# Performance work log

Hardware: AMD Instinct MI355X
Metric: run time of the kernel (lower is better)

## Reference

```python
import jax, jax.numpy as jnp
import numpy as np
from functools import partial

# Gate order along axis 0 of Wi/bi/Wh/bh: 0=r (input gate), 1=f (forget), 2=g (cell), 3=o (output)

def setup_inputs() -> dict:
    key = jax.random.key(0)
    ks = jax.random.split(key, 6)
    B, T, V, E, H, O = 64, 512, 32000, 256, 512, 1
    s_e, s_h = 1.0 / np.sqrt(E), 1.0 / np.sqrt(H)
    return {
        "input_words": jax.random.randint(ks[0], (B, T), 0, V, dtype=jnp.int64),
        "emb": jax.random.normal(ks[1], (V, E), dtype=jnp.float32) * 0.02,
        "Wi": jax.random.normal(ks[2], (4, H, E), dtype=jnp.float32) * s_e,
        "bi": jnp.zeros((4, H), dtype=jnp.float32),
        "Wh": jax.random.normal(ks[3], (4, H, H), dtype=jnp.float32) * s_h,
        "bh": jnp.zeros((4, H), dtype=jnp.float32),
        "Wfc": jax.random.normal(ks[4], (O, H), dtype=jnp.float32) * s_h,
        "bfc": jnp.zeros((O,), dtype=jnp.float32),
    }


def reference(input_words, emb, Wi, bi, Wh, bh, Wfc, bfc):
    B, T = input_words.shape
    H = Wh.shape[-1]
    x = emb[input_words]                     # [B, T, E]
    # Precompute input projections for all 4 gates, all timesteps: one big GEMM.
    xg = jnp.einsum('bte,ghe->tbgh', x, Wi) + bi  # [T, B, 4, H]

    def step(carry, xg_t):
        h, c = carry
        gates = xg_t + jnp.einsum('bk,ghk->bgh', h, Wh) + bh  # [B, 4, H]
        r = jax.nn.sigmoid(gates[:, 0])
        f = jax.nn.sigmoid(gates[:, 1])
        g = jnp.tanh(gates[:, 2])
        o = jax.nn.sigmoid(gates[:, 3])
        c = f * c + r * g
        h = o * jnp.tanh(c)
        return (h, c), None

    h0 = jnp.zeros((B, H), dtype=x.dtype)
    c0 = jnp.zeros((B, H), dtype=x.dtype)
    (h, c), _ = jax.lax.scan(step, (h0, c0), xg)
    out = jax.nn.sigmoid(h @ Wfc.T + bfc)    # [B, n_output]
    return (out, h)
```

## Files before the change

kernel.cpp:

```cpp
#include <hip/hip_runtime.h>
#include <hip/hip_bf16.h>

#define TB 512
#define NB 64
#define EE 256
#define HH 512
#define ND 8
#define DB 8
#define NBLK 8
#define NT 256
#define NCOLP 260
#define NPAIR 256
#define GCOLS 2048
#define SLOWOFF ((size_t)0x40000)
#define XGOFF   ((size_t)1 << 20)

typedef __bf16 bf16_t;
typedef bf16_t bf16x8 __attribute__((ext_vector_type(8)));
typedef float  f32x4  __attribute__((ext_vector_type(4)));
typedef unsigned u32;
typedef unsigned long long u64;
typedef u32 u32x4 __attribute__((ext_vector_type(4)));

__device__ __forceinline__ float sigf(float x) { return 1.0f / (1.0f + __expf(-x)); }
__device__ __forceinline__ float tanhfast(float x) {
    float xc = fminf(fmaxf(x, -15.0f), 15.0f);
    float e  = __expf(2.0f * xc);
    return (e - 1.0f) / (e + 1.0f);
}
__device__ __forceinline__ u32 bfbits(float f) {
    bf16_t h = (bf16_t)f;
    return (u32)__builtin_bit_cast(unsigned short, h);
}
__device__ __forceinline__ bf16x8 cvt8(float4 a, float4 b) {
    bf16x8 v;
    v[0]=(bf16_t)a.x; v[1]=(bf16_t)a.y; v[2]=(bf16_t)a.z; v[3]=(bf16_t)a.w;
    v[4]=(bf16_t)b.x; v[5]=(bf16_t)b.y; v[6]=(bf16_t)b.z; v[7]=(bf16_t)b.w;
    return v;
}
__device__ __forceinline__ f32x4 cvtxg(u64 v) {
    f32x4 r;
    r[0] = __uint_as_float((u32)( v        & 0xFFFFu) << 16);
    r[1] = __uint_as_float((u32)((v >> 16) & 0xFFFFu) << 16);
    r[2] = __uint_as_float((u32)((v >> 32) & 0xFFFFu) << 16);
    r[3] = __uint_as_float((u32)((v >> 48) & 0xFFFFu) << 16);
    return r;
}

__device__ __forceinline__ void poll8_dual(const u64* fsrc, const u64* ssrc,
                                           u32 tag, u64 (&pk)[4]) {
    u64 fa = (u64)fsrc;
    int it = 0;
    for (;;) {
        u32x4 q0, q1, q2, q3;
        asm volatile(
            "global_load_dwordx4 %0, %4, off sc0\n\t"
            "global_load_dwordx4 %1, %4, off offset:16 sc0\n\t"
            "global_load_dwordx4 %2, %4, off offset:32 sc0\n\t"
            "global_load_dwordx4 %3, %4, off offset:48 sc0\n\t"
            "s_waitcnt vmcnt(0)"
            : "=&v"(q0), "=&v"(q1), "=&v"(q2), "=&v"(q3)
            : "v"(fa)
            : "memory");
        if (q0[1]==tag && q0[3]==tag && q1[1]==tag && q1[3]==tag &&
            q2[1]==tag && q2[3]==tag && q3[1]==tag && q3[3]==tag) {
            pk[0] = (u64)q0[0] | ((u64)q0[2] << 32);
            pk[1] = (u64)q1[0] | ((u64)q1[2] << 32);
            pk[2] = (u64)q2[0] | ((u64)q2[2] << 32);
            pk[3] = (u64)q3[0] | ((u64)q3[2] << 32);
            return;
        }
        if (((++it) & 1) == 0) {
            u64 hv[8];
            #pragma unroll
            for (int j = 0; j < 8; ++j)
                hv[j] = __hip_atomic_load(ssrc + j, __ATOMIC_RELAXED, __HIP_MEMORY_SCOPE_AGENT);
            bool ok = true;
            #pragma unroll
            for (int j = 0; j < 8; ++j) ok &= ((u32)(hv[j] >> 32) == tag);
            if (ok) {
                #pragma unroll
                for (int k = 0; k < 4; ++k)
                    pk[k] = (u64)(u32)hv[2*k] | ((u64)(u32)hv[2*k + 1] << 32);
                return;
            }
        }
    }
}

__global__ __launch_bounds__(256, 1)
void xg_prepass(const int* __restrict__ words, const float* __restrict__ emb,
                const float* __restrict__ Wi, const float* __restrict__ bi,
                const float* __restrict__ bh, bf16_t* __restrict__ xgT)
{
    const int tid = threadIdx.x, lane = tid & 63, wv = tid >> 6;
    const int kgrp = lane >> 4, cl = lane & 15;
    const int cc = blockIdx.x & 7, tc = blockIdx.x >> 3;

    __shared__ __align__(16) bf16_t x_s[64][EE];

    bf16x8 wf[8][4];
    float  bv[4];
    #pragma unroll
    for (int nt = 0; nt < 4; ++nt) {
        int col = cc*256 + wv*64 + nt*16 + cl;
        int wrow = (col & 3)*HH + (col >> 2);
        const float* wr = Wi + (size_t)wrow*EE;
        #pragma unroll
        for (int kt = 0; kt < 8; ++kt) {
            const float4* p = (const float4*)(wr + kt*32 + kgrp*8);
            wf[kt][nt] = cvt8(p[0], p[1]);
        }
        bv[nt] = bi[wrow] + bh[wrow];
    }

    const int r0 = tid >> 2, q = tid & 3;
    const int swz = (r0 & 7) << 3;
    u64* dst = (u64*)xgT;

    for (int it = 0; it < 16; ++it) {
        int t = tc*16 + it;
        {
            int wd = words[r0*TB + t];
            const float4* p = (const float4*)(emb + (size_t)wd*EE + q*64);
            #pragma unroll
            for (int o = 0; o < 8; ++o) {
                float4 a = p[2*o], b2 = p[2*o + 1];
                *(bf16x8*)&x_s[r0][(q*64 + o*8) ^ swz] = cvt8(a, b2);
            }
        }
        __syncthreads();

        f32x4 acc[4][4];
        #pragma unroll
        for (int rt = 0; rt < 4; ++rt)
            #pragma unroll
            for (int nt = 0; nt < 4; ++nt)
                acc[rt][nt] = (f32x4){ bv[nt], bv[nt], bv[nt], bv[nt] };
        #pragma unroll
        for (int kt = 0; kt < 8; ++kt) {
            #pragma unroll
            for (int rt = 0; rt < 4; ++rt) {
                bf16x8 a = *(const bf16x8*)&x_s[rt*16 + cl][(kt*32 + kgrp*8) ^ ((cl & 7) << 3)];
                #pragma unroll
                for (int nt = 0; nt < 4; ++nt)
                    acc[rt][nt] = __builtin_amdgcn_mfma_f32_16x16x32_bf16(a, wf[kt][nt], acc[rt][nt], 0, 0, 0);
            }
        }
        #pragma unroll
        for (int nt = 0; nt < 4; ++nt) {
            int col = cc*256 + wv*64 + nt*16 + cl;
            #pragma unroll
            for (int rt = 0; rt < 4; ++rt) {
                f32x4 v = acc[rt][nt];
                u64 pkk =  (u64)(bfbits(v[0]))
                        | ((u64)(bfbits(v[1])) << 16)
                        | ((u64)(bfbits(v[2])) << 32)
                        | ((u64)(bfbits(v[3])) << 48);
                dst[(size_t)(t*GCOLS + col)*16 + rt*4 + kgrp] = pkk;
            }
        }
        __syncthreads();
    }
}

__global__ __launch_bounds__(NT, 1)
void lstm_main(const float* __restrict__ Wh,
               const float* __restrict__ Wfc,
               const float* __restrict__ bfc,
               float* __restrict__ out,
               u64* __restrict__ fastH,
               u64* __restrict__ slowH,
               const u64* __restrict__ xg64)
{
    const int tid  = threadIdx.x;
    const int lane = tid & 63;
    const int wv   = tid >> 6;
    const int g    = blockIdx.x >> 3;
    const int ug   = blockIdx.x & 7;
    const int kgrp = lane >> 4;
    const int cl   = lane & 15;

    __shared__ __align__(16) bf16_t h_lds[16][HH];
    __shared__ __align__(16) float  P_lds[16][NCOLP];

    for (int i = tid; i < 16*HH/2; i += NT) ((u32*)h_lds)[i] = 0u;

    bf16x8 whf[16][4];
    #pragma unroll
    for (int nt = 0; nt < 4; ++nt) {
        int gc = ug*256 + wv*64 + nt*16 + cl;
        int wrow = (gc & 3)*HH + (gc >> 2);
        const float* wr = Wh + (size_t)wrow*HH;
        #pragma unroll
        for (int kt = 0; kt < 16; ++kt) {
            const float4* p = (const float4*)(wr + kt*32 + kgrp*8);
            whf[kt][nt] = cvt8(p[0], p[1]);
        }
    }

    const int sb = tid >> 5, sc = tid & 31;
    const int swz = sb << 3;

    const int m = 2*g + (kgrp & 1);
    int gc[4];
    #pragma unroll
    for (int nt = 0; nt < 4; ++nt) gc[nt] = ug*256 + wv*64 + nt*16 + cl;

    u64 xgc[4], xgn[4];
    #pragma unroll
    for (int nt = 0; nt < 4; ++nt) xgc[nt] = xg64[(size_t)gc[nt]*16 + m];

    float c0 = 0.f, c1 = 0.f;
    __syncthreads();

    for (int t = 0; t < TB; ++t) {
        if (t > 0) {
            size_t off = ((size_t)((t & 1) ^ 1))*NB*NPAIR
                       + (size_t)(g*DB + sb)*NPAIR + sc*8;
            u64 pk[4];
            poll8_dual(fastH + off, slowH + off, (u32)t, pk);
            #pragma unroll
            for (int k = 0; k < 4; ++k) {
                int e = sc*16 + 4*k;
                int phys = ((e & ~7) ^ swz) | (e & 7);
                *(u64*)&h_lds[sb][phys] = pk[k];
            }
        }

        if (t + 1 < TB) {
            #pragma unroll
            for (int nt = 0; nt < 4; ++nt)
                xgn[nt] = xg64[(size_t)((t + 1)*GCOLS + gc[nt])*16 + m];
        }
        __syncthreads();

        f32x4 acc[4];
        #pragma unroll
        for (int nt = 0; nt < 4; ++nt) acc[nt] = cvtxg(xgc[nt]);
        if (t > 0) {
            #pragma unroll
            for (int kt = 0; kt < 16; ++kt) {
                bf16x8 a = *(const bf16x8*)&h_lds[cl][(kt*32 + kgrp*8) ^ ((cl & 7) << 3)];
                #pragma unroll
                for (int nt = 0; nt < 4; ++nt)
                    acc[nt] = __builtin_amdgcn_mfma_f32_16x16x32_bf16(a, whf[kt][nt], acc[nt], 0, 0, 0);
            }
        }

        #pragma unroll
        for (int nt = 0; nt < 4; ++nt)
            #pragma unroll
            for (int r = 0; r < 4; ++r)
                P_lds[kgrp*4 + r][wv*64 + nt*16 + cl] = acc[nt][r];
        __syncthreads();

        {
            float4 g0 = *(const float4*)&P_lds[sb][sc*8];
            float4 g1 = *(const float4*)&P_lds[sb][sc*8 + 4];
            float r0 = sigf(g0.x), f0 = sigf(g0.y), z0 = tanhfast(g0.z), o0 = sigf(g0.w);
            float r1 = sigf(g1.x), f1 = sigf(g1.y), z1 = tanhfast(g1.z), o1 = sigf(g1.w);
            c0 = f0*c0 + r0*z0;
            c1 = f1*c1 + r1*z1;
            float h0 = o0*tanhfast(c0);
            float h1 = o1*tanhfast(c1);
            if (t == TB - 1) {
                float2 hw = { h0, h1 };
                *(float2*)&out[64 + (size_t)(g*DB + sb)*HH + ug*64 + 2*sc] = hw;
            }
            u64 v = (((u64)(u32)(t + 1)) << 32)
                  | (u64)(bfbits(h0) | (bfbits(h1) << 16));
            size_t di = ((size_t)(t & 1))*NB*NPAIR
                      + (size_t)(g*DB + sb)*NPAIR + ug*32 + sc;
            asm volatile("global_store_dwordx2 %0, %1, off sc0"
                         :: "v"((u64)(fastH + di)), "v"(v) : "memory");
            __hip_atomic_store(slowH + di, v, __ATOMIC_RELAXED, __HIP_MEMORY_SCOPE_AGENT);
        }
        #pragma unroll
        for (int nt = 0; nt < 4; ++nt) xgc[nt] = xgn[nt];
    }

    if (ug == 0) {
        size_t off = ((size_t)((TB - 1) & 1))*NB*NPAIR
                   + (size_t)(g*DB + sb)*NPAIR + sc*8;
        u64 pk[4];
        poll8_dual(fastH + off, slowH + off, (u32)TB, pk);
        float s = 0.f;
        const float4* wp = (const float4*)(Wfc + sc*16);
        #pragma unroll
        for (int k = 0; k < 4; ++k) {
            float4 w = wp[k];
            u64 p = pk[k];
            s += __uint_as_float((u32)( p        & 0xFFFFu) << 16) * w.x;
            s += __uint_as_float((u32)((p >> 16) & 0xFFFFu) << 16) * w.y;
            s += __uint_as_float((u32)((p >> 32) & 0xFFFFu) << 16) * w.z;
            s += __uint_as_float((u32)((p >> 48) & 0xFFFFu) << 16) * w.w;
        }
        __syncthreads();
        P_lds[sb][sc] = s;
        __syncthreads();
        if (tid < 8) {
            float acc = 0.f;
            #pragma unroll
            for (int q = 0; q < 32; ++q) acc += P_lds[tid][q];
            out[g*DB + tid] = sigf(acc + bfc[0]);
        }
    }
}

extern "C" void kernel_launch(void* const* d_in, const int* in_sizes, int n_in,
                              void* d_out, int out_size, void* d_ws, size_t ws_size,
                              hipStream_t stream) {
    (void)in_sizes; (void)n_in; (void)out_size; (void)ws_size;
    const int*   words = (const int*)d_in[0];
    const float* emb   = (const float*)d_in[1];
    const float* Wi    = (const float*)d_in[2];
    const float* bi    = (const float*)d_in[3];
    const float* Wh    = (const float*)d_in[4];
    const float* bh    = (const float*)d_in[5];
    const float* Wfc   = (const float*)d_in[6];
    const float* bfc   = (const float*)d_in[7];
    float* out = (float*)d_out;

    u64* fastH  = (u64*)d_ws;
    u64* slowH  = (u64*)((char*)d_ws + SLOWOFF);
    bf16_t* xgT = (bf16_t*)((char*)d_ws + XGOFF);

    hipMemsetAsync(d_ws, 0, 2*SLOWOFF, stream);

    xg_prepass<<<dim3(256), dim3(256), 0, stream>>>(words, emb, Wi, bi, bh, xgT);
    lstm_main<<<dim3(ND*NBLK), dim3(NT), 0, stream>>>(Wh, Wfc, bfc, out,
                                                      fastH, slowH, (const u64*)xgT);
}
```

Before: 2.144 ms.

## Replace per-thread tagged polling with per-block sentinel flags polled by one wave

```diff
diff --git a/kernel.cpp b/kernel.cpp
--- a/kernel.cpp
+++ b/kernel.cpp
@@ -13,6 +13,7 @@
 #define NPAIR 256
 #define GCOLS 2048
 #define SLOWOFF ((size_t)0x40000)
+#define SENTOFF ((size_t)0x80000)
 #define XGOFF   ((size_t)1 << 20)
 
 typedef __bf16 bf16_t;
@@ -47,10 +48,9 @@
     return r;
 }
 
-__device__ __forceinline__ void poll8_dual(const u64* fsrc, const u64* ssrc,
-                                           u32 tag, u64 (&pk)[4]) {
+__device__ __forceinline__ void read8_tagged(const u64* fsrc, const u64* ssrc,
+                                             u32 tag, u64 (&pk)[4]) {
     u64 fa = (u64)fsrc;
-    int it = 0;
     for (;;) {
         u32x4 q0, q1, q2, q3;
         asm volatile(
@@ -70,20 +70,18 @@
             pk[3] = (u64)q3[0] | ((u64)q3[2] << 32);
             return;
         }
-        if (((++it) & 1) == 0) {
-            u64 hv[8];
-            #pragma unroll
-            for (int j = 0; j < 8; ++j)
-                hv[j] = __hip_atomic_load(ssrc + j, __ATOMIC_RELAXED, __HIP_MEMORY_SCOPE_AGENT);
-            bool ok = true;
-            #pragma unroll
-            for (int j = 0; j < 8; ++j) ok &= ((u32)(hv[j] >> 32) == tag);
-            if (ok) {
-                #pragma unroll
-                for (int k = 0; k < 4; ++k)
-                    pk[k] = (u64)(u32)hv[2*k] | ((u64)(u32)hv[2*k + 1] << 32);
-                return;
-            }
+        u64 hv[8];
+        #pragma unroll
+        for (int j = 0; j < 8; ++j)
+            hv[j] = __hip_atomic_load(ssrc + j, __ATOMIC_RELAXED, __HIP_MEMORY_SCOPE_AGENT);
+        bool ok = true;
+        #pragma unroll
+        for (int j = 0; j < 8; ++j) ok &= ((u32)(hv[j] >> 32) == tag);
+        if (ok) {
+            #pragma unroll
+            for (int k = 0; k < 4; ++k)
+                pk[k] = (u64)(u32)hv[2*k] | ((u64)(u32)hv[2*k + 1] << 32);
+            return;
         }
     }
 }
@@ -171,6 +169,7 @@
                float* __restrict__ out,
                u64* __restrict__ fastH,
                u64* __restrict__ slowH,
+               u64* __restrict__ sent,
                const u64* __restrict__ xg64)
 {
     const int tid  = threadIdx.x;
@@ -181,6 +180,9 @@
     const int kgrp = lane >> 4;
     const int cl   = lane & 15;
 
+    u64* sentF = sent;
+    u64* sentS = sent + 64*8;
+
     __shared__ __align__(16) bf16_t h_lds[16][HH];
     __shared__ __align__(16) float  P_lds[16][NCOLP];
 
@@ -216,10 +218,32 @@
 
     for (int t = 0; t < TB; ++t) {
         if (t > 0) {
+            if (wv == 0) {
+                const bool ml = (lane < 8);
+                const u64 sfa = (u64)(sentF + (size_t)(g*8 + (lane & 7))*8);
+                const u64* ssp = sentS + (size_t)(g*8 + (lane & 7))*8;
+                int it = 0;
+                for (;;) {
+                    u64 v = 0;
+                    if (ml) {
+                        if (it & 1) {
+                            asm volatile("global_load_dwordx2 %0, %1, off sc0\n\t"
+                                         "s_waitcnt vmcnt(0)"
+                                         : "=v"(v) : "v"(sfa) : "memory");
+                        } else {
+                            v = __hip_atomic_load(ssp, __ATOMIC_RELAXED, __HIP_MEMORY_SCOPE_AGENT);
+                        }
+                    }
+                    if (__all(ml ? (int)(v >= (u64)t) : 1)) break;
+                    ++it;
+                }
+            }
+            __syncthreads();
+
             size_t off = ((size_t)((t & 1) ^ 1))*NB*NPAIR
                        + (size_t)(g*DB + sb)*NPAIR + sc*8;
             u64 pk[4];
-            poll8_dual(fastH + off, slowH + off, (u32)t, pk);
+            read8_tagged(fastH + off, slowH + off, (u32)t, pk);
             #pragma unroll
             for (int k = 0; k < 4; ++k) {
                 int e = sc*16 + 4*k;
@@ -276,15 +300,48 @@
                          :: "v"((u64)(fastH + di)), "v"(v) : "memory");
             __hip_atomic_store(slowH + di, v, __ATOMIC_RELAXED, __HIP_MEMORY_SCOPE_AGENT);
         }
+
+        __builtin_amdgcn_sched_barrier(0);
+        asm volatile("s_waitcnt vmcnt(0)" ::: "memory");
+        __builtin_amdgcn_sched_barrier(0);
+        __syncthreads();
+        if (tid == NT - 1) {
+            u64 sv = (u64)(t + 1);
+            asm volatile("global_store_dwordx2 %0, %1, off sc0"
+                         :: "v"((u64)(sentF + (size_t)blockIdx.x*8)), "v"(sv) : "memory");
+            __hip_atomic_store(sentS + (size_t)blockIdx.x*8, sv,
+                               __ATOMIC_RELAXED, __HIP_MEMORY_SCOPE_AGENT);
+        }
         #pragma unroll
         for (int nt = 0; nt < 4; ++nt) xgc[nt] = xgn[nt];
     }
 
     if (ug == 0) {
+        if (wv == 0) {
+            const bool ml = (lane < 8);
+            const u64 sfa = (u64)(sentF + (size_t)(g*8 + (lane & 7))*8);
+            const u64* ssp = sentS + (size_t)(g*8 + (lane & 7))*8;
+            int it = 0;
+            for (;;) {
+                u64 v = 0;
+                if (ml) {
+                    if (it & 1) {
+                        asm volatile("global_load_dwordx2 %0, %1, off sc0\n\t"
+                                     "s_waitcnt vmcnt(0)"
+                                     : "=v"(v) : "v"(sfa) : "memory");
+                    } else {
+                        v = __hip_atomic_load(ssp, __ATOMIC_RELAXED, __HIP_MEMORY_SCOPE_AGENT);
+                    }
+                }
+                if (__all(ml ? (int)(v >= (u64)TB) : 1)) break;
+                ++it;
+            }
+        }
+        __syncthreads();
         size_t off = ((size_t)((TB - 1) & 1))*NB*NPAIR
                    + (size_t)(g*DB + sb)*NPAIR + sc*8;
         u64 pk[4];
-        poll8_dual(fastH + off, slowH + off, (u32)TB, pk);
+        read8_tagged(fastH + off, slowH + off, (u32)TB, pk);
         float s = 0.f;
         const float4* wp = (const float4*)(Wfc + sc*16);
         #pragma unroll
@@ -324,11 +381,12 @@
 
     u64* fastH  = (u64*)d_ws;
     u64* slowH  = (u64*)((char*)d_ws + SLOWOFF);
+    u64* sent   = (u64*)((char*)d_ws + SENTOFF);
     bf16_t* xgT = (bf16_t*)((char*)d_ws + XGOFF);
 
-    hipMemsetAsync(d_ws, 0, 2*SLOWOFF, stream);
+    hipMemsetAsync(d_ws, 0, SENTOFF + 2*64*8*sizeof(u64), stream);
 
     xg_prepass<<<dim3(256), dim3(256), 0, stream>>>(words, emb, Wi, bi, bh, xgT);
     lstm_main<<<dim3(ND*NBLK), dim3(NT), 0, stream>>>(Wh, Wfc, bfc, out,
-                                                      fastH, slowH, (const u64*)xgT);
-}
+                                                      fastH, slowH, sent, (const u64*)xgT);
+}
```

Result: slower. 2.521 ms (+17.6%).

## Load h fragments directly from global into MFMA operands, 16 batches per block

Applied to the files above, without the earlier changes.

```diff
diff --git a/kernel.cpp b/kernel.cpp
--- a/kernel.cpp
+++ b/kernel.cpp
@@ -5,8 +5,8 @@
 #define NB 64
 #define EE 256
 #define HH 512
-#define ND 8
-#define DB 8
+#define ND 4
+#define DB 16
 #define NBLK 8
 #define NT 256
 #define NCOLP 260
@@ -47,43 +47,56 @@
     return r;
 }
 
-__device__ __forceinline__ void poll8_dual(const u64* fsrc, const u64* ssrc,
-                                           u32 tag, u64 (&pk)[4]) {
-    u64 fa = (u64)fsrc;
-    int it = 0;
-    for (;;) {
-        u32x4 q0, q1, q2, q3;
-        asm volatile(
-            "global_load_dwordx4 %0, %4, off sc0\n\t"
-            "global_load_dwordx4 %1, %4, off offset:16 sc0\n\t"
-            "global_load_dwordx4 %2, %4, off offset:32 sc0\n\t"
-            "global_load_dwordx4 %3, %4, off offset:48 sc0\n\t"
-            "s_waitcnt vmcnt(0)"
-            : "=&v"(q0), "=&v"(q1), "=&v"(q2), "=&v"(q3)
-            : "v"(fa)
-            : "memory");
-        if (q0[1]==tag && q0[3]==tag && q1[1]==tag && q1[3]==tag &&
-            q2[1]==tag && q2[3]==tag && q3[1]==tag && q3[3]==tag) {
-            pk[0] = (u64)q0[0] | ((u64)q0[2] << 32);
-            pk[1] = (u64)q1[0] | ((u64)q1[2] << 32);
-            pk[2] = (u64)q2[0] | ((u64)q2[2] << 32);
-            pk[3] = (u64)q3[0] | ((u64)q3[2] << 32);
-            return;
-        }
-        if (((++it) & 1) == 0) {
-            u64 hv[8];
-            #pragma unroll
-            for (int j = 0; j < 8; ++j)
-                hv[j] = __hip_atomic_load(ssrc + j, __ATOMIC_RELAXED, __HIP_MEMORY_SCOPE_AGENT);
-            bool ok = true;
-            #pragma unroll
-            for (int j = 0; j < 8; ++j) ok &= ((u32)(hv[j] >> 32) == tag);
-            if (ok) {
-                #pragma unroll
-                for (int k = 0; k < 4; ++k)
-                    pk[k] = (u64)(u32)hv[2*k] | ((u64)(u32)hv[2*k + 1] << 32);
-                return;
-            }
+__device__ __forceinline__ void bar_lds() {
+    __builtin_amdgcn_sched_barrier(0);
+    asm volatile("s_waitcnt lgkmcnt(0)" ::: "memory");
+    __builtin_amdgcn_s_barrier();
+    __builtin_amdgcn_sched_barrier(0);
+}
+
+__device__ __forceinline__ void frag_issue(u64 fa, u32x4 (&q)[8]) {
+    asm volatile(
+        "global_load_dwordx4 %0, %8, off sc0\n\t"
+        "global_load_dwordx4 %1, %8, off offset:16 sc0\n\t"
+        "global_load_dwordx4 %2, %8, off offset:128 sc0\n\t"
+        "global_load_dwordx4 %3, %8, off offset:144 sc0\n\t"
+        "global_load_dwordx4 %4, %8, off offset:256 sc0\n\t"
+        "global_load_dwordx4 %5, %8, off offset:272 sc0\n\t"
+        "global_load_dwordx4 %6, %8, off offset:384 sc0\n\t"
+        "global_load_dwordx4 %7, %8, off offset:400 sc0"
+        : "=&v"(q[0]), "=&v"(q[1]), "=&v"(q[2]), "=&v"(q[3]),
+          "=&v"(q[4]), "=&v"(q[5]), "=&v"(q[6]), "=&v"(q[7])
+        : "v"(fa)
+        : "memory");
+}
+
+__device__ __forceinline__ bool frag_wait_ok(u32x4 (&q)[8], u32 tag) {
+    asm volatile("s_waitcnt vmcnt(0)"
+        : "+v"(q[0]), "+v"(q[1]), "+v"(q[2]), "+v"(q[3]),
+          "+v"(q[4]), "+v"(q[5]), "+v"(q[6]), "+v"(q[7])
+        :: "memory");
+    __builtin_amdgcn_sched_barrier(0);
+    bool ok = true;
+    #pragma unroll
+    for (int i = 0; i < 8; ++i) ok &= (q[i][1] == tag) & (q[i][3] == tag);
+    return ok;
+}
+
+__device__ __forceinline__ void frag_get(u64 fa, const u64* sb, u32 tag, u32x4 (&q)[8]) {
+    int round = 0;
+    while (!frag_wait_ok(q, tag)) {
+        if ((round++ & 1) == 0) {
+            #pragma unroll
+            for (int j = 0; j < 4; ++j) {
+                u64 h0 = __hip_atomic_load(sb + j*16 + 0, __ATOMIC_RELAXED, __HIP_MEMORY_SCOPE_AGENT);
+                u64 h1 = __hip_atomic_load(sb + j*16 + 1, __ATOMIC_RELAXED, __HIP_MEMORY_SCOPE_AGENT);
+                u64 h2 = __hip_atomic_load(sb + j*16 + 2, __ATOMIC_RELAXED, __HIP_MEMORY_SCOPE_AGENT);
+                u64 h3 = __hip_atomic_load(sb + j*16 + 3, __ATOMIC_RELAXED, __HIP_MEMORY_SCOPE_AGENT);
+                q[2*j]   = (u32x4){(u32)h0, (u32)(h0 >> 32), (u32)h1, (u32)(h1 >> 32)};
+                q[2*j+1] = (u32x4){(u32)h2, (u32)(h2 >> 32), (u32)h3, (u32)(h3 >> 32)};
+            }
+        } else {
+            frag_issue(fa, q);
         }
     }
 }
@@ -181,10 +194,7 @@
     const int kgrp = lane >> 4;
     const int cl   = lane & 15;
 
-    __shared__ __align__(16) bf16_t h_lds[16][HH];
-    __shared__ __align__(16) float  P_lds[16][NCOLP];
-
-    for (int i = tid; i < 16*HH/2; i += NT) ((u32*)h_lds)[i] = 0u;
+    __shared__ __align__(16) float P_lds[16][NCOLP];
 
     bf16x8 whf[16][4];
     #pragma unroll
@@ -199,52 +209,58 @@
         }
     }
 
-    const int sb = tid >> 5, sc = tid & 31;
-    const int swz = sb << 3;
-
-    const int m = 2*g + (kgrp & 1);
-    int gc[4];
-    #pragma unroll
-    for (int nt = 0; nt < 4; ++nt) gc[nt] = ug*256 + wv*64 + nt*16 + cl;
+    const int m = g*4 + kgrp;
+    int gcv[4];
+    #pragma unroll
+    for (int nt = 0; nt < 4; ++nt) gcv[nt] = ug*256 + wv*64 + nt*16 + cl;
 
     u64 xgc[4], xgn[4];
     #pragma unroll
-    for (int nt = 0; nt < 4; ++nt) xgc[nt] = xg64[(size_t)gc[nt]*16 + m];
-
-    float c0 = 0.f, c1 = 0.f;
+    for (int nt = 0; nt < 4; ++nt) xgc[nt] = xg64[(size_t)gcv[nt]*16 + m];
+
+    const int ab = tid >> 4, us = tid & 15;
+    float cs0 = 0.f, cs1 = 0.f, cs2 = 0.f, cs3 = 0.f;
+
     __syncthreads();
 
     for (int t = 0; t < TB; ++t) {
+        if (t + 1 < TB) {
+            #pragma unroll
+            for (int nt = 0; nt < 4; ++nt)
+                xgn[nt] = xg64[(size_t)((t + 1)*GCOLS + gcv[nt])*16 + m];
+        }
+
+        f32x4 acc[4];
+        #pragma unroll
+        for (int nt = 0; nt < 4; ++nt) acc[nt] = cvtxg(xgc[nt]);
+
         if (t > 0) {
-            size_t off = ((size_t)((t & 1) ^ 1))*NB*NPAIR
-                       + (size_t)(g*DB + sb)*NPAIR + sc*8;
-            u64 pk[4];
-            poll8_dual(fastH + off, slowH + off, (u32)t, pk);
-            #pragma unroll
-            for (int k = 0; k < 4; ++k) {
-                int e = sc*16 + 4*k;
-                int phys = ((e & ~7) ^ swz) | (e & 7);
-                *(u64*)&h_lds[sb][phys] = pk[k];
-            }
-        }
-
-        if (t + 1 < TB) {
-            #pragma unroll
-            for (int nt = 0; nt < 4; ++nt)
-                xgn[nt] = xg64[(size_t)((t + 1)*GCOLS + gc[nt])*16 + m];
-        }
-        __syncthreads();
-
-        f32x4 acc[4];
-        #pragma unroll
-        for (int nt = 0; nt < 4; ++nt) acc[nt] = cvtxg(xgc[nt]);
-        if (t > 0) {
-            #pragma unroll
-            for (int kt = 0; kt < 16; ++kt) {
-                bf16x8 a = *(const bf16x8*)&h_lds[cl][(kt*32 + kgrp*8) ^ ((cl & 7) << 3)];
+            size_t poff = ((size_t)((t & 1) ^ 1))*NB*NPAIR + (size_t)(g*DB + cl)*NPAIR;
+            const u64* fb  = fastH + poff;
+            const u64* sb2 = slowH + poff;
+            u32x4 q[8];
+            frag_issue((u64)fb*1 + (size_t)kgrp*32 + 0, q);
+            #pragma unroll
+            for (int grp = 0; grp < 4; ++grp) {
+                u64 fa = (u64)fb + (size_t)grp*512 + (size_t)kgrp*32;
+                frag_get(fa, sb2 + grp*64 + kgrp*4, (u32)t, q);
+                bf16x8 af[4];
+                union U { u32 w[4]; bf16x8 v; };
+                {
+                    U u0; u0.w[0]=q[0][0]; u0.w[1]=q[0][2]; u0.w[2]=q[1][0]; u0.w[3]=q[1][2]; af[0]=u0.v;
+                    U u1; u1.w[0]=q[2][0]; u1.w[1]=q[2][2]; u1.w[2]=q[3][0]; u1.w[3]=q[3][2]; af[1]=u1.v;
+                    U u2; u2.w[0]=q[4][0]; u2.w[1]=q[4][2]; u2.w[2]=q[5][0]; u2.w[3]=q[5][2]; af[2]=u2.v;
+                    U u3; u3.w[0]=q[6][0]; u3.w[1]=q[6][2]; u3.w[2]=q[7][0]; u3.w[3]=q[7][2]; af[3]=u3.v;
+                }
+                if (grp < 3)
+                    frag_issue((u64)fb + (size_t)(grp + 1)*512 + (size_t)kgrp*32, q);
                 #pragma unroll
-                for (int nt = 0; nt < 4; ++nt)
-                    acc[nt] = __builtin_amdgcn_mfma_f32_16x16x32_bf16(a, whf[kt][nt], acc[nt], 0, 0, 0);
+                for (int j = 0; j < 4; ++j) {
+                    int kt = grp*4 + j;
+                    #pragma unroll
+                    for (int nt = 0; nt < 4; ++nt)
+                        acc[nt] = __builtin_amdgcn_mfma_f32_16x16x32_bf16(af[j], whf[kt][nt], acc[nt], 0, 0, 0);
+                }
             }
         }
 
@@ -253,56 +269,72 @@
             #pragma unroll
             for (int r = 0; r < 4; ++r)
                 P_lds[kgrp*4 + r][wv*64 + nt*16 + cl] = acc[nt][r];
+        bar_lds();
+
+        {
+            float4 p0 = *(const float4*)&P_lds[ab][us*16 + 0];
+            float4 p1 = *(const float4*)&P_lds[ab][us*16 + 4];
+            float4 p2 = *(const float4*)&P_lds[ab][us*16 + 8];
+            float4 p3 = *(const float4*)&P_lds[ab][us*16 + 12];
+            float h0, h1, h2, h3;
+            { float r=sigf(p0.x), f=sigf(p0.y), z=tanhfast(p0.z), o=sigf(p0.w);
+              cs0 = f*cs0 + r*z; h0 = o*tanhfast(cs0); }
+            { float r=sigf(p1.x), f=sigf(p1.y), z=tanhfast(p1.z), o=sigf(p1.w);
+              cs1 = f*cs1 + r*z; h1 = o*tanhfast(cs1); }
+            { float r=sigf(p2.x), f=sigf(p2.y), z=tanhfast(p2.z), o=sigf(p2.w);
+              cs2 = f*cs2 + r*z; h2 = o*tanhfast(cs2); }
+            { float r=sigf(p3.x), f=sigf(p3.y), z=tanhfast(p3.z), o=sigf(p3.w);
+              cs3 = f*cs3 + r*z; h3 = o*tanhfast(cs3); }
+            if (t == TB - 1) {
+                float4 hw = { h0, h1, h2, h3 };
+                *(float4*)&out[64 + (size_t)(g*DB + ab)*HH + ug*64 + us*4] = hw;
+            }
+            u64 tg = ((u64)(u32)(t + 1)) << 32;
+            u64 v0 = tg | (u64)(bfbits(h0) | (bfbits(h1) << 16));
+            u64 v1 = tg | (u64)(bfbits(h2) | (bfbits(h3) << 16));
+            size_t di = ((size_t)(t & 1))*NB*NPAIR
+                      + (size_t)(g*DB + ab)*NPAIR + ug*32 + us*2;
+            asm volatile(
+                "global_store_dwordx2 %0, %1, off sc0\n\t"
+                "global_store_dwordx2 %0, %2, off offset:8 sc0"
+                :: "v"((u64)(fastH + di)), "v"(v0), "v"(v1) : "memory");
+            __hip_atomic_store(slowH + di,     v0, __ATOMIC_RELAXED, __HIP_MEMORY_SCOPE_AGENT);
+            __hip_atomic_store(slowH + di + 1, v1, __ATOMIC_RELAXED, __HIP_MEMORY_SCOPE_AGENT);
+        }
+        bar_lds();
+        #pragma unroll
+        for (int nt = 0; nt < 4; ++nt) xgc[nt] = xgn[nt];
+    }
+
+    if (ug == 0) {
         __syncthreads();
-
-        {
-            float4 g0 = *(const float4*)&P_lds[sb][sc*8];
-            float4 g1 = *(const float4*)&P_lds[sb][sc*8 + 4];
-            float r0 = sigf(g0.x), f0 = sigf(g0.y), z0 = tanhfast(g0.z), o0 = sigf(g0.w);
-            float r1 = sigf(g1.x), f1 = sigf(g1.y), z1 = tanhfast(g1.z), o1 = sigf(g1.w);
-            c0 = f0*c0 + r0*z0;
-            c1 = f1*c1 + r1*z1;
-            float h0 = o0*tanhfast(c0);
-            float h1 = o1*tanhfast(c1);
-            if (t == TB - 1) {
-                float2 hw = { h0, h1 };
-                *(float2*)&out[64 + (size_t)(g*DB + sb)*HH + ug*64 + 2*sc] = hw;
-            }
-            u64 v = (((u64)(u32)(t + 1)) << 32)
-                  | (u64)(bfbits(h0) | (bfbits(h1) << 16));
-            size_t di = ((size_t)(t & 1))*NB*NPAIR
-                      + (size_t)(g*DB + sb)*NPAIR + ug*32 + sc;
-            asm volatile("global_store_dwordx2 %0, %1, off sc0"
-                         :: "v"((u64)(fastH + di)), "v"(v) : "memory");
-            __hip_atomic_store(slowH + di, v, __ATOMIC_RELAXED, __HIP_MEMORY_SCOPE_AGENT);
-        }
-        #pragma unroll
-        for (int nt = 0; nt < 4; ++nt) xgc[nt] = xgn[nt];
-    }
-
-    if (ug == 0) {
-        size_t off = ((size_t)((TB - 1) & 1))*NB*NPAIR
-                   + (size_t)(g*DB + sb)*NPAIR + sc*8;
-        u64 pk[4];
-        poll8_dual(fastH + off, slowH + off, (u32)TB, pk);
+        int b = tid >> 4, seg = tid & 15;
+        const u64* sp = slowH + (size_t)1*NB*NPAIR + (size_t)(g*DB + b)*NPAIR + seg*16;
+        u64 hv[16];
+        for (;;) {
+            bool ok = true;
+            #pragma unroll
+            for (int j = 0; j < 16; ++j) {
+                hv[j] = __hip_atomic_load(sp + j, __ATOMIC_RELAXED, __HIP_MEMORY_SCOPE_AGENT);
+                ok &= ((u32)(hv[j] >> 32) == (u32)TB);
+            }
+            if (ok) break;
+            __builtin_amdgcn_s_sleep(1);
+        }
         float s = 0.f;
-        const float4* wp = (const float4*)(Wfc + sc*16);
-        #pragma unroll
-        for (int k = 0; k < 4; ++k) {
-            float4 w = wp[k];
-            u64 p = pk[k];
-            s += __uint_as_float((u32)( p        & 0xFFFFu) << 16) * w.x;
-            s += __uint_as_float((u32)((p >> 16) & 0xFFFFu) << 16) * w.y;
-            s += __uint_as_float((u32)((p >> 32) & 0xFFFFu) << 16) * w.z;
-            s += __uint_as_float((u32)((p >> 48) & 0xFFFFu) << 16) * w.w;
-        }
+        #pragma unroll
+        for (int j = 0; j < 16; ++j) {
+            u32 pl = (u32)hv[j];
+            int u = seg*32 + 2*j;
+            s += __uint_as_float((pl & 0xFFFFu) << 16) * Wfc[u];
+            s += __uint_as_float(pl & 0xFFFF0000u)     * Wfc[u + 1];
+        }
+        P_lds[b][seg] = s;
         __syncthreads();
-        P_lds[sb][sc] = s;
-        __syncthreads();
-        if (tid < 8) {
+        if (tid < 16) {
             float acc = 0.f;
             #pragma unroll
-            for (int q = 0; q < 32; ++q) acc += P_lds[tid][q];
+            for (int q2 = 0; q2 < 16; ++q2) acc += P_lds[tid][q2];
             out[g*DB + tid] = sigf(acc + bfc[0]);
         }
     }
```

Measured after the change: 6.497 ms. +203.0%, slower.

## Split LSTM block into compute and polling waves with double-buffered h

Applied to the files above, without the earlier changes.

```diff
diff --git a/kernel.cpp b/kernel.cpp
--- a/kernel.cpp
+++ b/kernel.cpp
@@ -8,7 +8,7 @@
 #define ND 8
 #define DB 8
 #define NBLK 8
-#define NT 256
+#define NT 512
 #define NCOLP 260
 #define NPAIR 256
 #define GCOLS 2048
@@ -45,6 +45,13 @@
     r[2] = __uint_as_float((u32)((v >> 32) & 0xFFFFu) << 16);
     r[3] = __uint_as_float((u32)((v >> 48) & 0xFFFFu) << 16);
     return r;
+}
+
+__device__ __forceinline__ void bar_lds() {
+    __builtin_amdgcn_sched_barrier(0);
+    asm volatile("s_waitcnt lgkmcnt(0)" ::: "memory");
+    __builtin_amdgcn_s_barrier();
+    __builtin_amdgcn_sched_barrier(0);
 }
 
 __device__ __forceinline__ void poll8_dual(const u64* fsrc, const u64* ssrc,
@@ -70,7 +77,7 @@
             pk[3] = (u64)q3[0] | ((u64)q3[2] << 32);
             return;
         }
-        if (((++it) & 1) == 0) {
+        if (((++it) & 3) == 0) {
             u64 hv[8];
             #pragma unroll
             for (int j = 0; j < 8; ++j)
@@ -176,20 +183,22 @@
     const int tid  = threadIdx.x;
     const int lane = tid & 63;
     const int wv   = tid >> 6;
+    const int wvm  = wv & 3;
     const int g    = blockIdx.x >> 3;
     const int ug   = blockIdx.x & 7;
     const int kgrp = lane >> 4;
     const int cl   = lane & 15;
-
-    __shared__ __align__(16) bf16_t h_lds[16][HH];
+    const bool cw  = (wv < 4);
+
+    __shared__ __align__(16) bf16_t h_lds[2][16][HH];
     __shared__ __align__(16) float  P_lds[16][NCOLP];
 
-    for (int i = tid; i < 16*HH/2; i += NT) ((u32*)h_lds)[i] = 0u;
+    for (int i = tid; i < 2*16*HH/2; i += NT) ((u32*)h_lds)[i] = 0u;
 
     bf16x8 whf[16][4];
     #pragma unroll
     for (int nt = 0; nt < 4; ++nt) {
-        int gc = ug*256 + wv*64 + nt*16 + cl;
+        int gc = ug*256 + wvm*64 + nt*16 + cl;
         int wrow = (gc & 3)*HH + (gc >> 2);
         const float* wr = Wh + (size_t)wrow*HH;
         #pragma unroll
@@ -199,63 +208,49 @@
         }
     }
 
-    const int sb = tid >> 5, sc = tid & 31;
-    const int swz = sb << 3;
+    const int sb = (tid >> 5) & 7, sc = tid & 31;
+    const int io  = tid - 256;
+    const int iob = (io >> 5) & 7, ioc = io & 31;
+    const int ioswz = (iob & 7) << 3;
 
     const int m = 2*g + (kgrp & 1);
-    int gc[4];
+    int gcv[4];
     #pragma unroll
-    for (int nt = 0; nt < 4; ++nt) gc[nt] = ug*256 + wv*64 + nt*16 + cl;
-
-    u64 xgc[4], xgn[4];
-    #pragma unroll
-    for (int nt = 0; nt < 4; ++nt) xgc[nt] = xg64[(size_t)gc[nt]*16 + m];
+    for (int nt = 0; nt < 4; ++nt) gcv[nt] = ug*256 + wvm*64 + nt*16 + cl;
+
+    u64 xgc[4] = {0,0,0,0}, xgn[4] = {0,0,0,0};
+    if (cw) {
+        #pragma unroll
+        for (int nt = 0; nt < 4; ++nt) xgc[nt] = xg64[(size_t)gcv[nt]*16 + m];
+    }
 
     float c0 = 0.f, c1 = 0.f;
     __syncthreads();
 
     for (int t = 0; t < TB; ++t) {
-        if (t > 0) {
-            size_t off = ((size_t)((t & 1) ^ 1))*NB*NPAIR
-                       + (size_t)(g*DB + sb)*NPAIR + sc*8;
-            u64 pk[4];
-            poll8_dual(fastH + off, slowH + off, (u32)t, pk);
-            #pragma unroll
-            for (int k = 0; k < 4; ++k) {
-                int e = sc*16 + 4*k;
-                int phys = ((e & ~7) ^ swz) | (e & 7);
-                *(u64*)&h_lds[sb][phys] = pk[k];
-            }
-        }
-
-        if (t + 1 < TB) {
+        if (cw) {
+            f32x4 acc[4];
+            #pragma unroll
+            for (int nt = 0; nt < 4; ++nt) acc[nt] = cvtxg(xgc[nt]);
+            if (t > 0) {
+                const bf16_t (*hb)[HH] = h_lds[(t & 1) ^ 1];
+                #pragma unroll
+                for (int kt = 0; kt < 16; ++kt) {
+                    bf16x8 a = *(const bf16x8*)&hb[cl][(kt*32 + kgrp*8) ^ ((cl & 7) << 3)];
+                    #pragma unroll
+                    for (int nt = 0; nt < 4; ++nt)
+                        acc[nt] = __builtin_amdgcn_mfma_f32_16x16x32_bf16(a, whf[kt][nt], acc[nt], 0, 0, 0);
+                }
+            }
             #pragma unroll
             for (int nt = 0; nt < 4; ++nt)
-                xgn[nt] = xg64[(size_t)((t + 1)*GCOLS + gc[nt])*16 + m];
-        }
-        __syncthreads();
-
-        f32x4 acc[4];
-        #pragma unroll
-        for (int nt = 0; nt < 4; ++nt) acc[nt] = cvtxg(xgc[nt]);
-        if (t > 0) {
-            #pragma unroll
-            for (int kt = 0; kt < 16; ++kt) {
-                bf16x8 a = *(const bf16x8*)&h_lds[cl][(kt*32 + kgrp*8) ^ ((cl & 7) << 3)];
-                #pragma unroll
-                for (int nt = 0; nt < 4; ++nt)
-                    acc[nt] = __builtin_amdgcn_mfma_f32_16x16x32_bf16(a, whf[kt][nt], acc[nt], 0, 0, 0);
-            }
-        }
-
-        #pragma unroll
-        for (int nt = 0; nt < 4; ++nt)
-            #pragma unroll
-            for (int r = 0; r < 4; ++r)
-                P_lds[kgrp*4 + r][wv*64 + nt*16 + cl] = acc[nt][r];
-        __syncthreads();
-
-        {
+                #pragma unroll
+                for (int r = 0; r < 4; ++r)
+                    P_lds[kgrp*4 + r][wvm*64 + nt*16 + cl] = acc[nt][r];
+        }
+        bar_lds();
+
+        if (cw) {
             float4 g0 = *(const float4*)&P_lds[sb][sc*8];
             float4 g1 = *(const float4*)&P_lds[sb][sc*8 + 4];
             float r0 = sigf(g0.x), f0 = sigf(g0.y), z0 = tanhfast(g0.z), o0 = sigf(g0.w);
@@ -275,34 +270,63 @@
             asm volatile("global_store_dwordx2 %0, %1, off sc0"
                          :: "v"((u64)(fastH + di)), "v"(v) : "memory");
             __hip_atomic_store(slowH + di, v, __ATOMIC_RELAXED, __HIP_MEMORY_SCOPE_AGENT);
-        }
-        #pragma unroll
-        for (int nt = 0; nt < 4; ++nt) xgc[nt] = xgn[nt];
+            if (t + 1 < TB) {
+                #pragma unroll
+                for (int nt = 0; nt < 4; ++nt)
+                    xgn[nt] = xg64[(size_t)((t + 1)*GCOLS + gcv[nt])*16 + m];
+            }
+            #pragma unroll
+            for (int nt = 0; nt < 4; ++nt) xgc[nt] = xgn[nt];
+        } else if (t + 1 < TB) {
+            size_t off = ((size_t)(t & 1))*NB*NPAIR
+                       + (size_t)(g*DB + iob)*NPAIR + ioc*8;
+            u64 pk[4];
+            poll8_dual(fastH + off, slowH + off, (u32)(t + 1), pk);
+            #pragma unroll
+            for (int k = 0; k < 4; ++k) {
+                int e = ioc*16 + 4*k;
+                int phys = ((e & ~7) ^ ioswz) | (e & 7);
+                *(u64*)&h_lds[t & 1][iob][phys] = pk[k];
+            }
+        }
+        bar_lds();
     }
 
     if (ug == 0) {
-        size_t off = ((size_t)((TB - 1) & 1))*NB*NPAIR
-                   + (size_t)(g*DB + sb)*NPAIR + sc*8;
-        u64 pk[4];
-        poll8_dual(fastH + off, slowH + off, (u32)TB, pk);
         float s = 0.f;
-        const float4* wp = (const float4*)(Wfc + sc*16);
-        #pragma unroll
-        for (int k = 0; k < 4; ++k) {
-            float4 w = wp[k];
-            u64 p = pk[k];
-            s += __uint_as_float((u32)( p        & 0xFFFFu) << 16) * w.x;
-            s += __uint_as_float((u32)((p >> 16) & 0xFFFFu) << 16) * w.y;
-            s += __uint_as_float((u32)((p >> 32) & 0xFFFFu) << 16) * w.z;
-            s += __uint_as_float((u32)((p >> 48) & 0xFFFFu) << 16) * w.w;
+        if (tid < 256) {
+            const u64* sp = slowH + ((size_t)((TB - 1) & 1))*NB*NPAIR
+                          + (size_t)(g*DB + sb)*NPAIR + sc*8;
+            u64 hv[8];
+            for (;;) {
+                bool ok = true;
+                #pragma unroll
+                for (int j = 0; j < 8; ++j) {
+                    hv[j] = __hip_atomic_load(sp + j, __ATOMIC_RELAXED, __HIP_MEMORY_SCOPE_AGENT);
+                    ok &= ((u32)(hv[j] >> 32) == (u32)TB);
+                }
+                if (ok) break;
+                __builtin_amdgcn_s_sleep(1);
+            }
+            const float4* wp = (const float4*)(Wfc + sc*16);
+            #pragma unroll
+            for (int k = 0; k < 4; ++k) {
+                float4 w = wp[k];
+                u64 p = hv[2*k] | 0ull;
+                u64 p2 = hv[2*k + 1];
+                s += __uint_as_float((u32)( p        & 0xFFFFu) << 16) * w.x;
+                s += __uint_as_float((u32)((p >> 16) & 0xFFFFu) << 16) * w.y;
+                s += __uint_as_float((u32)( p2        & 0xFFFFu) << 16) * w.z;
+                s += __uint_as_float((u32)((p2 >> 16) & 0xFFFFu) << 16) * w.w;
+            }
         }
         __syncthreads();
-        P_lds[sb][sc] = s;
+        if (tid < 256) P_lds[sb][sc] = s;
         __syncthreads();
         if (tid < 8) {
             float acc = 0.f;
             #pragma unroll
-            for (int q = 0; q < 32; ++q) acc += P_lds[tid][q];
+            for (int q2 = 0; q2 < 32; ++q2) acc += P_lds[tid][q2];
             out[g*DB + tid] = sigf(acc + bfc[0]);
         }
     }
```

Result: slower. 3.381 ms (+57.7%).
